# Performance work log

Hardware: AMD Instinct MI355X
Metric: run time of the kernel (lower is better)

Reference implementation:

```python
import jax, jax.numpy as jnp
import numpy as np

B, N, D, E, C = 8, 4096, 1024, 512, 4096


def setup_inputs() -> dict:
    key = jax.random.key(0)
    k1, k2, k3 = jax.random.split(key, 3)
    x = jax.random.normal(k1, (B, N, D), dtype=jnp.float32)
    # xavier_normal_ scale for an (input_dim, codebook_dim) matrix
    scale = (2.0 / (D + E)) ** 0.5
    random_projection = jax.random.normal(k2, (D, E), dtype=jnp.float32) * scale
    codebook = jax.random.normal(k3, (C, E), dtype=jnp.float32)
    return {"x": x, "random_projection": random_projection, "codebook": codebook}


def _l2norm(v, eps=1e-12):
    # matches torch.nn.functional.normalize(p=2): v / max(||v||, eps)
    return v / jnp.maximum(jnp.linalg.norm(v, axis=-1, keepdims=True), eps)


def reference(x, random_projection, codebook):
    # project: b n d, d e -> b n e
    proj = jnp.einsum("bnd,de->bne", x, random_projection)
    pn = _l2norm(proj)            # [B, N, E], unit vectors
    cn = _l2norm(codebook)        # [C, E],   unit vectors
    # For unit vectors, ||p - c||^2 = 2 - 2 * <p, c>, so
    # argmin_c cdist == argmax_c cosine similarity (same indices as torch code).
    sim = jnp.einsum("bne,ce->bnc", pn, cn)  # [B, N, C]
    xq = jnp.argmax(sim, axis=-1).astype(jnp.int32)  # [B, N]
    return xq
```

## Files before the change

### kernel.cpp

```cpp
#include <hip/hip_runtime.h>
#include <math.h>


typedef _Float16 half8 __attribute__((ext_vector_type(8)));
typedef _Float16 half4 __attribute__((ext_vector_type(4)));
typedef float f32x4 __attribute__((ext_vector_type(4)));
typedef unsigned long long u64;
typedef unsigned int u32;

#define INV2048 (4.8828125e-4f)
#define MARGIN 0.03f

struct Split { _Float16 h, l; };

__device__ __forceinline__ Split split_f32(float v) {
    Split s;
    s.h = (_Float16)v;
    s.l = (_Float16)((v - (float)s.h) * 2048.0f);
    return s;
}

__device__ __forceinline__ void gl_lds16(const void* g, void* l) {
    __builtin_amdgcn_global_load_lds(
        (const __attribute__((address_space(1))) unsigned int*)g,
        (__attribute__((address_space(3))) unsigned int*)l, 16, 0, 0);
}

__device__ __forceinline__ u32 fkey(float v) {
    u32 b = __float_as_uint(v);
    return b ^ ((u32)((int)b >> 31) | 0x80000000u);
}
__device__ __forceinline__ float fkeyinv(u32 u) {
    u32 m2 = (u32)((int)u >> 31);
    return __uint_as_float(u ^ ((~m2) | 0x80000000u));
}

__global__ __launch_bounds__(256) void k_prep(const float* __restrict__ rp,
                                              _Float16* __restrict__ th,
                                              _Float16* __restrict__ tl,
                                              const float* __restrict__ cb,
                                              _Float16* __restrict__ ch,
                                              _Float16* __restrict__ cl,
                                              int* __restrict__ cnt) {
    const int t = threadIdx.x;
    if (blockIdx.x == 0 && t == 0) *cnt = 0;
    if (blockIdx.x < 128) {
        __shared__ float tile[64][65];
        const int k0 = (blockIdx.x & 15) * 64, n0 = (blockIdx.x >> 4) * 64;
        const int rr = t >> 6, cc = t & 63;
        #pragma unroll
        for (int i = 0; i < 16; ++i) {
            int r = i * 4 + rr;
            tile[r][cc] = rp[(size_t)(k0 + r) * 512 + n0 + cc];
        }
        __syncthreads();
        #pragma unroll
        for (int i = 0; i < 16; ++i) {
            int n = i * 4 + rr;
            Split s = split_f32(tile[cc][n]);
            size_t o = (size_t)(n0 + n) * 1024 + k0 + cc;
            th[o] = s.h;
            tl[o] = s.l;
        }
    } else {
        const int c = blockIdx.x - 128;
        const float* row = cb + (size_t)c * 512;
        float v0 = row[t];
        float v1 = row[t + 256];
        float ss = v0 * v0 + v1 * v1;
        #pragma unroll
        for (int o = 32; o > 0; o >>= 1) ss += __shfl_down(ss, o, 64);
        __shared__ float wsum[4];
        if ((t & 63) == 0) wsum[t >> 6] = ss;
        __syncthreads();
        float s = 1.0f / fmaxf(sqrtf(wsum[0] + wsum[1] + wsum[2] + wsum[3]), 1e-12f);
        Split s0 = split_f32(v0 * s);
        ch[(size_t)c * 512 + t] = s0.h;
        cl[(size_t)c * 512 + t] = s0.l;
        Split s1 = split_f32(v1 * s);
        ch[(size_t)c * 512 + t + 256] = s1.h;
        cl[(size_t)c * 512 + t + 256] = s1.l;
    }
}

__global__ __launch_bounds__(256, 2) void k_gemm1(const float* __restrict__ X,
                                                  const _Float16* __restrict__ Bh,
                                                  const _Float16* __restrict__ Bl,
                                                  _Float16* __restrict__ Ph,
                                                  _Float16* __restrict__ Pl) {
    __shared__ _Float16 sAh[128 * 64], sAl[128 * 64];
    __shared__ _Float16 sBh[128 * 64], sBl[128 * 64];
    const int t = threadIdx.x;
    const int nb = blockIdx.x;
    const int mb = blockIdx.y;
    const int lane = t & 63, w = t >> 6;
    const int quad = lane >> 4, l15 = lane & 15;
    const int wm = w >> 1, wn = w & 1;

    f32x4 acc[4][4], acc2[4][4];
    const f32x4 z = {0.f, 0.f, 0.f, 0.f};
    #pragma unroll
    for (int i = 0; i < 4; ++i)
        #pragma unroll
        for (int j = 0; j < 4; ++j) { acc[i][j] = z; acc2[i][j] = z; }

    const int srow8 = lane >> 3;
    const int sseg = (lane & 7) ^ srow8;
    const _Float16* gBh = Bh + (size_t)(nb * 128 + w * 32 + srow8) * 1024 + sseg * 8;
    const _Float16* gBl = Bl + (size_t)(nb * 128 + w * 32 + srow8) * 1024 + sseg * 8;

    const int xrow = t >> 1;
    const int xk8 = (t & 1) * 4;
    const float* gX = X + (size_t)(mb * 128 + xrow) * 1024 + xk8 * 8;
    _Float16* wAh = &sAh[xrow * 64];
    _Float16* wAl = &sAl[xrow * 64];
    const int xswz = xrow & 7;

    for (int ks = 0; ks < 16; ++ks) {
        const int ko = ks * 64;
        __syncthreads();
        #pragma unroll
        for (int c = 0; c < 4; ++c) {
            gl_lds16(gBh + ko + (size_t)(c * 8) * 1024, &sBh[(w * 32 + c * 8) * 64]);
            gl_lds16(gBl + ko + (size_t)(c * 8) * 1024, &sBl[(w * 32 + c * 8) * 64]);
        }
        #pragma unroll
        for (int j = 0; j < 4; ++j) {
            float4 v0 = *(const float4*)(gX + ko + j * 8);
            float4 v1 = *(const float4*)(gX + ko + j * 8 + 4);
            Split s0 = split_f32(v0.x), s1 = split_f32(v0.y);
            Split s2 = split_f32(v0.z), s3 = split_f32(v0.w);
            Split s4 = split_f32(v1.x), s5 = split_f32(v1.y);
            Split s6 = split_f32(v1.z), s7 = split_f32(v1.w);
            half8 hv, lv;
            hv[0] = s0.h; hv[1] = s1.h; hv[2] = s2.h; hv[3] = s3.h;
            hv[4] = s4.h; hv[5] = s5.h; hv[6] = s6.h; hv[7] = s7.h;
            lv[0] = s0.l; lv[1] = s1.l; lv[2] = s2.l; lv[3] = s3.l;
            lv[4] = s4.l; lv[5] = s5.l; lv[6] = s6.l; lv[7] = s7.l;
            const int slot = ((xk8 + j) ^ xswz) * 8;
            *(half8*)&wAh[slot] = hv;
            *(half8*)&wAl[slot] = lv;
        }
        __syncthreads();
        #pragma unroll
        for (int phase = 0; phase < 2; ++phase) {
            const int slot = (((phase << 2) | quad) ^ (l15 & 7)) * 8;
            half8 ah[4], al[4], bh[4], bl[4];
            #pragma unroll
            for (int i = 0; i < 4; ++i) {
                ah[i] = *(const half8*)&sAh[(wm * 64 + i * 16 + l15) * 64 + slot];
                al[i] = *(const half8*)&sAl[(wm * 64 + i * 16 + l15) * 64 + slot];
                bh[i] = *(const half8*)&sBh[(wn * 64 + i * 16 + l15) * 64 + slot];
                bl[i] = *(const half8*)&sBl[(wn * 64 + i * 16 + l15) * 64 + slot];
            }
            #pragma unroll
            for (int mi = 0; mi < 4; ++mi)
                #pragma unroll
                for (int ni = 0; ni < 4; ++ni) {
                    acc[mi][ni]  = __builtin_amdgcn_mfma_f32_16x16x32_f16(ah[mi], bh[ni], acc[mi][ni], 0, 0, 0);
                    acc2[mi][ni] = __builtin_amdgcn_mfma_f32_16x16x32_f16(ah[mi], bl[ni], acc2[mi][ni], 0, 0, 0);
                    acc2[mi][ni] = __builtin_amdgcn_mfma_f32_16x16x32_f16(al[mi], bh[ni], acc2[mi][ni], 0, 0, 0);
                }
        }
    }
    #pragma unroll
    for (int mi = 0; mi < 4; ++mi)
        #pragma unroll
        for (int r = 0; r < 4; ++r) {
            int row = mb * 128 + wm * 64 + mi * 16 + quad * 4 + r;
            #pragma unroll
            for (int ni = 0; ni < 4; ++ni) {
                int col = nb * 128 + wn * 64 + ni * 16 + l15;
                float v = acc[mi][ni][r] + acc2[mi][ni][r] * INV2048;
                Split s = split_f32(v);
                Ph[(size_t)row * 512 + col] = s.h;
                Pl[(size_t)row * 512 + col] = s.l;
            }
        }
}

__global__ __launch_bounds__(256, 2) void k_sim_h(const _Float16* __restrict__ Ah,
                                                  const _Float16* __restrict__ Bh,
                                                  float* __restrict__ pv1,
                                                  int* __restrict__ pi1,
                                                  float* __restrict__ pv2) {
    __shared__ __align__(16) long long smem64[6144];
    _Float16* sA = (_Float16*)smem64;
    _Float16* sB = sA + 128 * 64;
    u64* ept = (u64*)smem64;
    u32* epv = (u32*)((char*)smem64 + 32768);
    const int t = threadIdx.x;
    const int cbk = blockIdx.x;
    const int mb = blockIdx.y;
    const int lane = t & 63, w = t >> 6;
    const int quad = lane >> 4, l15 = lane & 15;
    const int wm = w >> 1, wn = w & 1;

    f32x4 acc[4][8];
    const f32x4 z = {0.f, 0.f, 0.f, 0.f};
    #pragma unroll
    for (int i = 0; i < 4; ++i)
        #pragma unroll
        for (int j = 0; j < 8; ++j) acc[i][j] = z;

    const int srow8 = lane >> 3;
    const int sseg = (lane & 7) ^ srow8;
    const _Float16* gA = Ah + (size_t)(mb * 128 + w * 32 + srow8) * 512 + sseg * 8;
    const _Float16* gB = Bh + (size_t)(cbk * 256 + w * 64 + srow8) * 512 + sseg * 8;

    for (int ks = 0; ks < 8; ++ks) {
        const int ko = ks * 64;
        __syncthreads();
        #pragma unroll
        for (int c = 0; c < 4; ++c)
            gl_lds16(gA + ko + (size_t)(c * 8) * 512, &sA[(w * 32 + c * 8) * 64]);
        #pragma unroll
        for (int c = 0; c < 8; ++c)
            gl_lds16(gB + ko + (size_t)(c * 8) * 512, &sB[(w * 64 + c * 8) * 64]);
        __syncthreads();
        #pragma unroll
        for (int phase = 0; phase < 2; ++phase) {
            const int slot = (((phase << 2) | quad) ^ (l15 & 7)) * 8;
            half8 a[4], b[8];
            #pragma unroll
            for (int i = 0; i < 4; ++i)
                a[i] = *(const half8*)&sA[(wm * 64 + i * 16 + l15) * 64 + slot];
            #pragma unroll
            for (int j = 0; j < 8; ++j)
                b[j] = *(const half8*)&sB[(wn * 128 + j * 16 + l15) * 64 + slot];
            #pragma unroll
            for (int mi = 0; mi < 4; ++mi)
                #pragma unroll
                for (int ni = 0; ni < 8; ++ni)
                    acc[mi][ni] = __builtin_amdgcn_mfma_f32_16x16x32_f16(a[mi], b[ni], acc[mi][ni], 0, 0, 0);
        }
    }

    __syncthreads();
    #pragma unroll
    for (int mi = 0; mi < 4; ++mi)
        #pragma unroll
        for (int r = 0; r < 4; ++r) {
            int row = wm * 64 + mi * 16 + quad * 4 + r;
            u64 p1 = 0, p2 = 0;
            #pragma unroll
            for (int ni = 0; ni < 8; ++ni) {
                float v = acc[mi][ni][r];
                u32 col = cbk * 256 + wn * 128 + ni * 16 + l15;
                u64 p = ((u64)fkey(v) << 32) | (u32)(~col);
                if (p > p1) { p2 = p1; p1 = p; }
                else if (p > p2) p2 = p;
            }
            int e = row * 32 + wn * 16 + l15;
            ept[e] = p1;
            epv[e] = (u32)(p2 >> 32);
        }
    __syncthreads();
    if (t < 128) {
        u64 b1 = 0, b2 = 0;
        u32 vk2 = 0;
        #pragma unroll
        for (int jj = 0; jj < 32; ++jj) {
            int j = (jj + t) & 31;
            u64 p = ept[t * 32 + j];
            if (p > b1) { b2 = b1; b1 = p; }
            else if (p > b2) b2 = p;
            u32 vk = epv[t * 32 + j];
            vk2 = vk > vk2 ? vk : vk2;
        }
        u32 k2 = (u32)(b2 >> 32);
        if (vk2 > k2) k2 = vk2;
        size_t o = (size_t)(mb * 128 + t) * 16 + cbk;
        pv1[o] = fkeyinv((u32)(b1 >> 32));
        pi1[o] = (int)(~(u32)b1);
        pv2[o] = fkeyinv(k2);
    }
}

__global__ __launch_bounds__(256) void k_flag(const float* __restrict__ pv1,
                                              const int* __restrict__ pi1,
                                              const float* __restrict__ pv2,
                                              int* __restrict__ out,
                                              int* __restrict__ list,
                                              int* __restrict__ cnt) {
    int r = blockIdx.x * 256 + threadIdx.x;
    if (r >= 32768) return;
    size_t base = (size_t)r * 16;
    float v1 = pv1[base], v2 = pv2[base];
    int i1 = pi1[base];
    #pragma unroll
    for (int j = 1; j < 16; ++j) {
        float ov1 = pv1[base + j], ov2 = pv2[base + j];
        int oi1 = pi1[base + j];
        if (ov1 > v1 || (ov1 == v1 && oi1 < i1)) { v2 = fmaxf(v1, ov2); v1 = ov1; i1 = oi1; }
        else v2 = fmaxf(v2, ov1);
    }
    out[r] = i1;
    if (v1 - v2 < MARGIN) {
        int p = atomicAdd(cnt, 1);
        list[p] = r;
    }
}

__global__ __launch_bounds__(256, 2) void k_sim_fix(const _Float16* __restrict__ Ah,
                                                    const _Float16* __restrict__ Al,
                                                    const _Float16* __restrict__ Bh,
                                                    const _Float16* __restrict__ Bl,
                                                    const int* __restrict__ list,
                                                    const int* __restrict__ cnt,
                                                    float* __restrict__ rpv,
                                                    int* __restrict__ rpi) {
    __shared__ _Float16 sAh[128 * 32], sAl[128 * 32], sBh[128 * 32], sBl[128 * 32];
    __shared__ int rowidx[128];
    __shared__ float pvs[128][2];
    __shared__ int   pis[128][2];
    const int count = *cnt;
    const int t = threadIdx.x;
    const int cbk = blockIdx.x;
    const int lane = t & 63, w = t >> 6;
    const int quad = lane >> 4, l15 = lane & 15;
    const int wm = w >> 1, wn = w & 1;

    const int srow = w * 32 + (lane >> 2);
    const int kcol = (lane & 3) * 8;
    const _Float16* gBh = Bh + (size_t)(cbk * 128 + srow) * 512 + kcol;
    const _Float16* gBl = Bl + (size_t)(cbk * 128 + srow) * 512 + kcol;

    for (int g = blockIdx.y; g * 128 < count; g += gridDim.y) {
        __syncthreads();
        if (t < 128) {
            int p = g * 128 + t;
            rowidx[t] = (p < count) ? list[p] : list[0];
        }
        __syncthreads();

        f32x4 acc[4][4], acc2[4][4];
        const f32x4 z = {0.f, 0.f, 0.f, 0.f};
        #pragma unroll
        for (int i = 0; i < 4; ++i)
            #pragma unroll
            for (int j = 0; j < 4; ++j) { acc[i][j] = z; acc2[i][j] = z; }

        for (int ks = 0; ks < 16; ++ks) {
            const int ko = ks * 32;
            __syncthreads();
            gl_lds16(gBh + ko, &sBh[w * 1024]);
            gl_lds16(gBh + ko + (size_t)16 * 512, &sBh[w * 1024 + 512]);
            gl_lds16(gBl + ko, &sBl[w * 1024]);
            gl_lds16(gBl + ko + (size_t)16 * 512, &sBl[w * 1024 + 512]);
            #pragma unroll
            for (int i = 0; i < 2; ++i) {
                int idx = i * 256 + t;
                int row = idx >> 2, seg = (idx & 3) * 8;
                size_t src = (size_t)rowidx[row] * 512 + ko + seg;
                *(half8*)&sAh[row * 32 + seg] = *(const half8*)(Ah + src);
                *(half8*)&sAl[row * 32 + seg] = *(const half8*)(Al + src);
            }
            __syncthreads();
            half8 ah[4], al[4], bh[4], bl[4];
            #pragma unroll
            for (int i = 0; i < 4; ++i) {
                ah[i] = *(const half8*)&sAh[(wm * 64 + i * 16 + l15) * 32 + quad * 8];
                al[i] = *(const half8*)&sAl[(wm * 64 + i * 16 + l15) * 32 + quad * 8];
                bh[i] = *(const half8*)&sBh[(wn * 64 + i * 16 + l15) * 32 + quad * 8];
                bl[i] = *(const half8*)&sBl[(wn * 64 + i * 16 + l15) * 32 + quad * 8];
            }
            #pragma unroll
            for (int mi = 0; mi < 4; ++mi)
                #pragma unroll
                for (int ni = 0; ni < 4; ++ni) {
                    acc[mi][ni]  = __builtin_amdgcn_mfma_f32_16x16x32_f16(ah[mi], bh[ni], acc[mi][ni], 0, 0, 0);
                    acc2[mi][ni] = __builtin_amdgcn_mfma_f32_16x16x32_f16(ah[mi], bl[ni], acc2[mi][ni], 0, 0, 0);
                    acc2[mi][ni] = __builtin_amdgcn_mfma_f32_16x16x32_f16(al[mi], bh[ni], acc2[mi][ni], 0, 0, 0);
                }
        }

        #pragma unroll
        for (int mi = 0; mi < 4; ++mi)
            #pragma unroll
            for (int r = 0; r < 4; ++r) {
                float bv = -INFINITY;
                int bi = 0x7fffffff;
                #pragma unroll
                for (int ni = 0; ni < 4; ++ni) {
                    float v = acc[mi][ni][r] + acc2[mi][ni][r] * INV2048;
                    int col = cbk * 128 + wn * 64 + ni * 16 + l15;
                    if (v > bv || (v == bv && col < bi)) { bv = v; bi = col; }
                }
                #pragma unroll
                for (int o = 1; o < 16; o <<= 1) {
                    float ov = __shfl_xor(bv, o, 64);
                    int oi = __shfl_xor(bi, o, 64);
                    if (ov > bv || (ov == bv && oi < bi)) { bv = ov; bi = oi; }
                }
                if (l15 == 0) {
                    int row = wm * 64 + mi * 16 + quad * 4 + r;
                    pvs[row][wn] = bv; pis[row][wn] = bi;
                }
            }
        __syncthreads();
        if (t < 128 && g * 128 + t < count) {
            float v0 = pvs[t][0], v1 = pvs[t][1];
            int i0 = pis[t][0], i1 = pis[t][1];
            bool sw = (v1 > v0) || (v1 == v0 && i1 < i0);
            size_t o = (size_t)(g * 128 + t) * 32 + cbk;
            rpv[o] = sw ? v1 : v0;
            rpi[o] = sw ? i1 : i0;
        }
    }
}

__global__ __launch_bounds__(256) void k_fix(const float* __restrict__ rpv,
                                             const int* __restrict__ rpi,
                                             const int* __restrict__ list,
                                             const int* __restrict__ cnt,
                                             int* __restrict__ out) {
    int p = blockIdx.x * 256 + threadIdx.x;
    if (p >= *cnt) return;
    size_t base = (size_t)p * 32;
    float bv = -INFINITY;
    int bi = 0x7fffffff;
    #pragma unroll
    for (int j = 0; j < 32; ++j) {
        float v = rpv[base + j];
        int ci = rpi[base + j];
        if (v > bv || (v == bv && ci < bi)) { bv = v; bi = ci; }
    }
    out[list[p]] = bi;
}

extern "C" void kernel_launch(void* const* d_in, const int* in_sizes, int n_in,
                              void* d_out, int out_size, void* d_ws, size_t ws_size,
                              hipStream_t stream) {
    const float* x  = (const float*)d_in[0];
    const float* rp = (const float*)d_in[1];
    const float* cb = (const float*)d_in[2];
    int* out = (int*)d_out;

    char* ws = (char*)d_ws;
    _Float16* cn_h   = (_Float16*)(ws);
    _Float16* cn_l   = (_Float16*)(ws + ((size_t)4 << 20));
    _Float16* rpT_h  = (_Float16*)(ws + ((size_t)8 << 20));
    _Float16* rpT_l  = (_Float16*)(ws + ((size_t)9 << 20));
    _Float16* proj_h = (_Float16*)(ws + ((size_t)10 << 20));
    _Float16* proj_l = (_Float16*)(ws + ((size_t)42 << 20));
    float*    pv1    = (float*)   (ws + ((size_t)74 << 20));
    int*      pi1    = (int*)     (ws + ((size_t)78 << 20));
    float*    pv2    = (float*)   (ws + ((size_t)82 << 20));
    float*    rpv    = (float*)   (ws + ((size_t)86 << 20));
    int*      rpi    = (int*)     (ws + ((size_t)90 << 20));
    int*      list   = (int*)     (ws + ((size_t)94 << 20));
    int*      cnt    = (int*)     (ws + ((size_t)94 << 20) + (128 << 10));

    k_prep<<<4224, 256, 0, stream>>>(rp, rpT_h, rpT_l, cb, cn_h, cn_l, cnt);
    k_gemm1<<<dim3(4, 256), 256, 0, stream>>>(x, rpT_h, rpT_l, proj_h, proj_l);
    k_sim_h<<<dim3(16, 256), 256, 0, stream>>>(proj_h, cn_h, pv1, pi1, pv2);
    k_flag<<<128, 256, 0, stream>>>(pv1, pi1, pv2, out, list, cnt);
    k_sim_fix<<<dim3(32, 32), 256, 0, stream>>>(proj_h, proj_l, cn_h, cn_l, list, cnt, rpv, rpi);
    k_fix<<<128, 256, 0, stream>>>(rpv, rpi, list, cnt, out);
}
```

Baseline: 552.7 us.

## Double-buffer 256x256 sim GEMM tiles with 8 waves and shuffle-reduced epilogue

The similarity GEMM now uses 512-thread blocks over 256x256 tiles with double-buffered LDS. Each k-slice is split into four quarter phases that interleave global-to-LDS prefetch with MFMA work, using s_setprio and explicit barriers. The top-2 epilogue reduces across lanes with xor shuffles instead of a wide LDS scan. The projection GEMM grid is flattened with a block-index swizzle that groups the four N-blocks of each M-block onto one XCD for cache locality. This adds LDS footprint (64KB) and barrier count, and may reduce occupancy.

```diff
diff --git a/kernel.cpp b/kernel.cpp
--- a/kernel.cpp
+++ b/kernel.cpp
@@ -91,8 +91,10 @@
     __shared__ _Float16 sAh[128 * 64], sAl[128 * 64];
     __shared__ _Float16 sBh[128 * 64], sBl[128 * 64];
     const int t = threadIdx.x;
-    const int nb = blockIdx.x;
-    const int mb = blockIdx.y;
+    const int bid = blockIdx.x;
+    const int logical = (bid & 7) * 128 + (bid >> 3);
+    const int nb = logical & 3;
+    const int mb = logical >> 2;
     const int lane = t & 63, w = t >> 6;
     const int quad = lane >> 4, l15 = lane & 15;
     const int wm = w >> 1, wn = w & 1;
@@ -179,98 +181,148 @@
         }
 }
 
-__global__ __launch_bounds__(256, 2) void k_sim_h(const _Float16* __restrict__ Ah,
+__global__ __launch_bounds__(512, 2) void k_sim_h(const _Float16* __restrict__ Ah,
                                                   const _Float16* __restrict__ Bh,
                                                   float* __restrict__ pv1,
                                                   int* __restrict__ pi1,
                                                   float* __restrict__ pv2) {
-    __shared__ __align__(16) long long smem64[6144];
-    _Float16* sA = (_Float16*)smem64;
-    _Float16* sB = sA + 128 * 64;
-    u64* ept = (u64*)smem64;
-    u32* epv = (u32*)((char*)smem64 + 32768);
+    __shared__ __align__(16) _Float16 sA[2][256 * 64];
+    __shared__ __align__(16) _Float16 sB[2][256 * 64];
+    u64* ept = (u64*)&sA[0][0];
+    u32* epv = (u32*)&sB[0][0];
     const int t = threadIdx.x;
     const int cbk = blockIdx.x;
     const int mb = blockIdx.y;
     const int lane = t & 63, w = t >> 6;
     const int quad = lane >> 4, l15 = lane & 15;
-    const int wm = w >> 1, wn = w & 1;
-
-    f32x4 acc[4][8];
+    const int wm = w >> 2, wn = w & 3;
+
+    f32x4 acc[8][4];
     const f32x4 z = {0.f, 0.f, 0.f, 0.f};
     #pragma unroll
-    for (int i = 0; i < 4; ++i)
-        #pragma unroll
-        for (int j = 0; j < 8; ++j) acc[i][j] = z;
+    for (int i = 0; i < 8; ++i)
+        #pragma unroll
+        for (int j = 0; j < 4; ++j) acc[i][j] = z;
 
     const int srow8 = lane >> 3;
     const int sseg = (lane & 7) ^ srow8;
-    const _Float16* gA = Ah + (size_t)(mb * 128 + w * 32 + srow8) * 512 + sseg * 8;
-    const _Float16* gB = Bh + (size_t)(cbk * 256 + w * 64 + srow8) * 512 + sseg * 8;
-
-    for (int ks = 0; ks < 8; ++ks) {
-        const int ko = ks * 64;
-        __syncthreads();
-        #pragma unroll
-        for (int c = 0; c < 4; ++c)
-            gl_lds16(gA + ko + (size_t)(c * 8) * 512, &sA[(w * 32 + c * 8) * 64]);
-        #pragma unroll
-        for (int c = 0; c < 8; ++c)
-            gl_lds16(gB + ko + (size_t)(c * 8) * 512, &sB[(w * 64 + c * 8) * 64]);
-        __syncthreads();
-        #pragma unroll
-        for (int phase = 0; phase < 2; ++phase) {
-            const int slot = (((phase << 2) | quad) ^ (l15 & 7)) * 8;
-            half8 a[4], b[8];
+    const _Float16* gA = Ah + (size_t)(mb * 256 + w * 32 + srow8) * 512 + sseg * 8;
+    const _Float16* gB = Bh + (size_t)(cbk * 256 + w * 32 + srow8) * 512 + sseg * 8;
+
+    #pragma unroll
+    for (int c = 0; c < 4; ++c) {
+        gl_lds16(gA + (size_t)(c * 8) * 512, &sA[0][(w * 32 + c * 8) * 64]);
+        gl_lds16(gB + (size_t)(c * 8) * 512, &sB[0][(w * 32 + c * 8) * 64]);
+    }
+
+    for (int kt = 0; kt < 8; ++kt) {
+        const int cur = kt & 1;
+        const _Float16* rA = &sA[cur][0];
+        const _Float16* rB = &sB[cur][0];
+        _Float16* pA = &sA[cur ^ 1][0];
+        _Float16* pB = &sB[cur ^ 1][0];
+        const size_t konext = (size_t)(kt + 1) * 64;
+
+        asm volatile("s_waitcnt vmcnt(0)" ::: "memory");
+        __builtin_amdgcn_s_barrier();
+        asm volatile("" ::: "memory");
+
+        half8 a[4][2], b[2][2];
+        const int mh_[4] = {0, 0, 1, 1};
+        const int nh_[4] = {0, 1, 1, 0};
+        #pragma unroll
+        for (int q = 0; q < 4; ++q) {
+            const int mh = mh_[q], nh = nh_[q];
+            if (q == 0 || q == 2) {
+                #pragma unroll
+                for (int i = 0; i < 4; ++i)
+                    #pragma unroll
+                    for (int kh = 0; kh < 2; ++kh)
+                        a[i][kh] = *(const half8*)&rA[(wm * 128 + mh * 64 + i * 16 + l15) * 64
+                                                     + ((((kh << 2) | quad) ^ (l15 & 7)) << 3)];
+            }
+            if (q != 2) {
+                #pragma unroll
+                for (int j = 0; j < 2; ++j)
+                    #pragma unroll
+                    for (int kh = 0; kh < 2; ++kh)
+                        b[j][kh] = *(const half8*)&rB[(wn * 64 + nh * 32 + j * 16 + l15) * 64
+                                                     + ((((kh << 2) | quad) ^ (l15 & 7)) << 3)];
+            }
+            if (kt < 7 && q < 2) {
+                #pragma unroll
+                for (int cc = 0; cc < 2; ++cc) {
+                    const int c = q * 2 + cc;
+                    gl_lds16(gA + konext + (size_t)(c * 8) * 512, &pA[(w * 32 + c * 8) * 64]);
+                    gl_lds16(gB + konext + (size_t)(c * 8) * 512, &pB[(w * 32 + c * 8) * 64]);
+                }
+            }
+            asm volatile("" ::: "memory");
+            __builtin_amdgcn_s_barrier();
+            asm volatile("s_waitcnt lgkmcnt(0)" ::: "memory");
+            __builtin_amdgcn_sched_barrier(0);
+            __builtin_amdgcn_s_setprio(1);
             #pragma unroll
             for (int i = 0; i < 4; ++i)
-                a[i] = *(const half8*)&sA[(wm * 64 + i * 16 + l15) * 64 + slot];
-            #pragma unroll
-            for (int j = 0; j < 8; ++j)
-                b[j] = *(const half8*)&sB[(wn * 128 + j * 16 + l15) * 64 + slot];
-            #pragma unroll
-            for (int mi = 0; mi < 4; ++mi)
-                #pragma unroll
-                for (int ni = 0; ni < 8; ++ni)
-                    acc[mi][ni] = __builtin_amdgcn_mfma_f32_16x16x32_f16(a[mi], b[ni], acc[mi][ni], 0, 0, 0);
+                #pragma unroll
+                for (int j = 0; j < 2; ++j)
+                    #pragma unroll
+                    for (int kh = 0; kh < 2; ++kh)
+                        acc[mh * 4 + i][nh * 2 + j] =
+                            __builtin_amdgcn_mfma_f32_16x16x32_f16(a[i][kh], b[j][kh],
+                                                                   acc[mh * 4 + i][nh * 2 + j], 0, 0, 0);
+            __builtin_amdgcn_s_setprio(0);
+            if (q < 3) {
+                asm volatile("" ::: "memory");
+                __builtin_amdgcn_s_barrier();
+            }
         }
     }
 
     __syncthreads();
     #pragma unroll
-    for (int mi = 0; mi < 4; ++mi)
+    for (int mi = 0; mi < 8; ++mi)
         #pragma unroll
         for (int r = 0; r < 4; ++r) {
-            int row = wm * 64 + mi * 16 + quad * 4 + r;
             u64 p1 = 0, p2 = 0;
             #pragma unroll
-            for (int ni = 0; ni < 8; ++ni) {
+            for (int ni = 0; ni < 4; ++ni) {
                 float v = acc[mi][ni][r];
-                u32 col = cbk * 256 + wn * 128 + ni * 16 + l15;
+                u32 col = cbk * 256 + wn * 64 + ni * 16 + l15;
                 u64 p = ((u64)fkey(v) << 32) | (u32)(~col);
                 if (p > p1) { p2 = p1; p1 = p; }
                 else if (p > p2) p2 = p;
             }
-            int e = row * 32 + wn * 16 + l15;
-            ept[e] = p1;
-            epv[e] = (u32)(p2 >> 32);
+            #pragma unroll
+            for (int m = 1; m < 16; m <<= 1) {
+                u64 q1 = __shfl_xor(p1, m, 64);
+                u64 q2 = __shfl_xor(p2, m, 64);
+                u64 lo = p1 < q1 ? p1 : q1;
+                p1 = p1 < q1 ? q1 : p1;
+                p2 = p2 < q2 ? q2 : p2;
+                p2 = p2 < lo ? lo : p2;
+            }
+            if (l15 == 0) {
+                int rloc = wm * 128 + mi * 16 + quad * 4 + r;
+                ept[rloc * 4 + wn] = p1;
+                epv[rloc * 4 + wn] = (u32)(p2 >> 32);
+            }
         }
     __syncthreads();
-    if (t < 128) {
+    if (t < 256) {
         u64 b1 = 0, b2 = 0;
         u32 vk2 = 0;
         #pragma unroll
-        for (int jj = 0; jj < 32; ++jj) {
-            int j = (jj + t) & 31;
-            u64 p = ept[t * 32 + j];
+        for (int j = 0; j < 4; ++j) {
+            u64 p = ept[t * 4 + j];
             if (p > b1) { b2 = b1; b1 = p; }
             else if (p > b2) b2 = p;
-            u32 vk = epv[t * 32 + j];
+            u32 vk = epv[t * 4 + j];
             vk2 = vk > vk2 ? vk : vk2;
         }
         u32 k2 = (u32)(b2 >> 32);
         if (vk2 > k2) k2 = vk2;
-        size_t o = (size_t)(mb * 128 + t) * 16 + cbk;
+        size_t o = (size_t)(mb * 256 + t) * 16 + cbk;
         pv1[o] = fkeyinv((u32)(b1 >> 32));
         pi1[o] = (int)(~(u32)b1);
         pv2[o] = fkeyinv(k2);
@@ -453,8 +505,8 @@
     int*      cnt    = (int*)     (ws + ((size_t)94 << 20) + (128 << 10));
 
     k_prep<<<4224, 256, 0, stream>>>(rp, rpT_h, rpT_l, cb, cn_h, cn_l, cnt);
-    k_gemm1<<<dim3(4, 256), 256, 0, stream>>>(x, rpT_h, rpT_l, proj_h, proj_l);
-    k_sim_h<<<dim3(16, 256), 256, 0, stream>>>(proj_h, cn_h, pv1, pi1, pv2);
+    k_gemm1<<<1024, 256, 0, stream>>>(x, rpT_h, rpT_l, proj_h, proj_l);
+    k_sim_h<<<dim3(16, 128), 512, 0, stream>>>(proj_h, cn_h, pv1, pi1, pv2);
     k_flag<<<128, 256, 0, stream>>>(pv1, pi1, pv2, out, list, cnt);
     k_sim_fix<<<dim3(32, 32), 256, 0, stream>>>(proj_h, proj_l, cn_h, cn_l, list, cnt, rpv, rpi);
     k_fix<<<128, 256, 0, stream>>>(rpv, rpi, list, cnt, out);
```

After: 610.4 us. 10.4% more time.
